# Kernel tuning notes

Hardware: AMD Instinct MI355X
Metric: run time of the kernel (lower is better)

## Reference

```python
import jax, jax.numpy as jnp
import numpy as np
import math

HEAD_DIM = 128
N_HEADS = 32
N_KV_HEADS = 8
ROPE_THETA = 10000.0


def _rotate_half(x):
    x1, x2 = jnp.split(x, 2, axis=-1)
    return jnp.concatenate([-x2, x1], axis=-1)


def _rope_cos_sin(position_ids, head_dim, theta):
    # position_ids: [B, S] int
    inv_freq = 1.0 / (theta ** (jnp.arange(0, head_dim, 2, dtype=jnp.float32) / head_dim))
    freqs = position_ids.astype(jnp.float32)[..., None] * inv_freq[None, None, :]  # [B,S,D/2]
    emb = jnp.concatenate([freqs, freqs], axis=-1)  # [B,S,D]
    return jnp.cos(emb), jnp.sin(emb)


def setup_inputs() -> dict:
    key = jax.random.key(0)
    k1, k2, k3, k4, k5 = jax.random.split(key, 5)
    B, S, H = 1, 2048, 4096
    hidden_states = jax.random.normal(k1, (B, S, H), dtype=jnp.float32)
    Wq = jax.random.normal(k2, (N_HEADS * HEAD_DIM, H), dtype=jnp.float32) * (1.0 / math.sqrt(H))
    Wk = jax.random.normal(k3, (N_KV_HEADS * HEAD_DIM, H), dtype=jnp.float32) * (1.0 / math.sqrt(H))
    Wv = jax.random.normal(k4, (N_KV_HEADS * HEAD_DIM, H), dtype=jnp.float32) * (1.0 / math.sqrt(H))
    Wo = jax.random.normal(k5, (H, N_HEADS * HEAD_DIM), dtype=jnp.float32) * (1.0 / math.sqrt(H))
    position_ids = jnp.arange(S, dtype=jnp.int32)[None, :]
    return {"hidden_states": hidden_states, "Wq": Wq, "Wk": Wk, "Wv": Wv, "Wo": Wo,
            "position_ids": position_ids}


def reference(hidden_states, Wq, Wk, Wv, Wo, position_ids):
    B, S, H = hidden_states.shape
    d = HEAD_DIM
    groups = N_HEADS // N_KV_HEADS

    # projections (torch Linear: x @ W^T)
    q = (hidden_states @ Wq.T).reshape(B, S, N_HEADS, d).transpose(0, 2, 1, 3)      # [B,Hq,S,d]
    k = (hidden_states @ Wk.T).reshape(B, S, N_KV_HEADS, d).transpose(0, 2, 1, 3)   # [B,Hk,S,d]
    v = (hidden_states @ Wv.T).reshape(B, S, N_KV_HEADS, d).transpose(0, 2, 1, 3)

    cos, sin = _rope_cos_sin(position_ids, d, ROPE_THETA)  # [B,S,d]
    cos = cos[:, None, :, :]
    sin = sin[:, None, :, :]
    q = q * cos + _rotate_half(q) * sin
    k = k * cos + _rotate_half(k) * sin

    # GQA: repeat kv heads
    k = jnp.repeat(k, groups, axis=1)  # [B,Hq,S,d]
    v = jnp.repeat(v, groups, axis=1)

    scores = jnp.einsum('bhqd,bhkd->bhqk', q, k) / math.sqrt(d)
    causal = jnp.tril(jnp.ones((S, S), dtype=bool))
    scores = jnp.where(causal[None, None], scores, jnp.finfo(jnp.float32).min)
    attn = jax.nn.softmax(scores.astype(jnp.float32), axis=-1).astype(q.dtype)

    out = jnp.einsum('bhqk,bhkd->bhqd', attn, v)        # [B,Hq,S,d]
    out = out.transpose(0, 2, 1, 3).reshape(B, S, N_HEADS * d)
    return out @ Wo.T
```

## Files before the change

kernel.cpp:

```cpp
#include <hip/hip_runtime.h>
#include <hip/hip_bf16.h>
#include <cstdint>
#include <cstddef>

#define S_LEN 2048
#define HID   4096
#define HD    128
#define NH    32
#define NKV   8
#define KVW   (NKV * HD)
#define QKVN  (HID + 2 * KVW)

typedef __bf16 bf16x8_t __attribute__((ext_vector_type(8)));
typedef float  f32x4_t  __attribute__((ext_vector_type(4)));
typedef unsigned short u16x8_t __attribute__((ext_vector_type(8)));

__device__ __forceinline__ unsigned short f2b(float f) {
  unsigned u = __float_as_uint(f);
  u += 0x7FFFu + ((u >> 16) & 1u);
  return (unsigned short)(u >> 16);
}
__device__ __forceinline__ float b2f(unsigned short v) {
  return __uint_as_float(((unsigned)v) << 16);
}
__device__ __forceinline__ void gld_lds16(const void* g, void* l) {
  __builtin_amdgcn_global_load_lds(
      (const __attribute__((address_space(1))) void*)g,
      (__attribute__((address_space(3))) void*)l, 16, 0, 0);
}

__global__ void cvt_kernel(const float* __restrict__ src,
                           unsigned short* __restrict__ dst, int n4) {
  int i = blockIdx.x * blockDim.x + threadIdx.x;
  int stride = gridDim.x * blockDim.x;
  for (; i < n4; i += stride) {
    float4 v = reinterpret_cast<const float4*>(src)[i];
    ushort4 o;
    o.x = f2b(v.x); o.y = f2b(v.y); o.z = f2b(v.z); o.w = f2b(v.w);
    reinterpret_cast<ushort4*>(dst)[i] = o;
  }
}

__global__ void rope_kernel(unsigned short* __restrict__ Q,
                            unsigned short* __restrict__ Kb,
                            const int* __restrict__ pos_ids) {
  const int total = S_LEN * (NH + NKV) * 64;
  int idx = blockIdx.x * blockDim.x + threadIdx.x;
  int stride = gridDim.x * blockDim.x;
  for (; idx < total; idx += stride) {
    int s   = idx / ((NH + NKV) * 64);
    int rem = idx % ((NH + NKV) * 64);
    int hp  = rem >> 6;
    int i   = rem & 63;
    unsigned short* ptr; int W, h;
    if (hp < NH) { ptr = Q;  W = HID; h = hp; }
    else         { ptr = Kb; W = KVW; h = hp - NH; }
    float pos = (float)pos_ids[s];
    float ang = pos * __expf(-(float)i * 0.14391156516f);
    float sn, cs;
    sincosf(ang, &sn, &cs);
    size_t base = (size_t)s * W + (size_t)h * HD + i;
    float lo = b2f(ptr[base]);
    float hi = b2f(ptr[base + 64]);
    ptr[base]      = f2b(lo * cs - hi * sn);
    ptr[base + 64] = f2b(hi * cs + lo * sn);
  }
}

template <int BM, int MODE>
__global__ __launch_bounds__(512, 2) void gemm8p_kernel(
    const unsigned short* __restrict__ A, const unsigned short* __restrict__ B,
    void* __restrict__ C0, void* __restrict__ C1, void* __restrict__ C2,
    int N, int K) {
  constexpr int BN = 256;
  constexpr int PWM = BM / 2;
  constexpr int MFR = PWM / 16;
  constexpr int MPP = MFR / 4;
  constexpr int ABYTES = BM * 128;
  constexpr int TILE_LDS = ABYTES + BN * 128;
  constexpr int A_UNITS = ABYTES / 8192;
  constexpr int TUNITS = A_UNITS + 4;
  constexpr int VM_N = TUNITS - 2;
  __shared__ char ldsB[2 * TILE_LDS];

  const int tid  = threadIdx.x;
  const int lane = tid & 63;
  const int wid  = tid >> 6;
  const int wm = wid >> 2, wn = wid & 3;
  const int lr = lane & 15, g = lane >> 4;

  const int gx = gridDim.x;
  const int nwg = gx * gridDim.y;
  const int lin = blockIdx.y * gx + blockIdx.x;
  const int swz = (lin & 7) * (nwg >> 3) + (lin >> 3);
  const int bm = (swz / gx) * BM;
  const int bn = (swz % gx) * BN;

  const int nk = K >> 6;
  const int ni = nk >> 1;
  const int xr = (lr & 7) << 4;

  auto stage_u = [&](int t, int u) {
    if (t >= nk) return;
    const int riu = tid >> 3;
    const int cbs = ((tid & 7) << 4) ^ ((riu & 7) << 4);
    const char* src;
    if (u < A_UNITS)
      src = (const char*)A + ((size_t)(bm + u * 64 + riu) * K + t * 64) * 2 + cbs;
    else
      src = (const char*)B + ((size_t)(bn + (u - A_UNITS) * 64 + riu) * K + t * 64) * 2 + cbs;
    gld_lds16(src, ldsB + (t & 1) * TILE_LDS + u * 8192 + tid * 16);
  };

  auto rdA = [&](const char* bb, int m, int k) {
    const int row = wm * PWM + m * 16 + lr;
    return *(const bf16x8_t*)(bb + row * 128 + ((k * 64 + g * 16) ^ xr));
  };
  auto rdB = [&](const char* bb, int n, int k) {
    const int row = wn * 64 + n * 16 + lr;
    return *(const bf16x8_t*)(bb + ABYTES + row * 128 + ((k * 64 + g * 16) ^ xr));
  };

  for (int t = 0; t < 2; ++t)
    for (int u = 0; u < TUNITS; ++u) stage_u(t, u);
  asm volatile("s_waitcnt vmcnt(0)" ::: "memory");
  __builtin_amdgcn_sched_barrier(0);
  __builtin_amdgcn_s_barrier();

  f32x4_t acc[MFR][4];
#pragma unroll
  for (int m = 0; m < MFR; ++m)
#pragma unroll
    for (int n = 0; n < 4; ++n) acc[m][n] = f32x4_t{0.f, 0.f, 0.f, 0.f};

  bf16x8_t bfr[4][2], af[MPP][2];

#define MFMA_BLOCK(MB)                                                        \
  __builtin_amdgcn_s_setprio(1);                                              \
  _Pragma("unroll") for (int m = 0; m < MPP; ++m)                             \
    _Pragma("unroll") for (int n = 0; n < 4; ++n)                             \
      _Pragma("unroll") for (int k = 0; k < 2; ++k)                           \
        acc[(MB) + m][n] = __builtin_amdgcn_mfma_f32_16x16x32_bf16(           \
            af[m][k], bfr[n][k], acc[(MB) + m][n], 0, 0, 0);                  \
  __builtin_amdgcn_s_setprio(0);

#define GATE()                                                                \
  __builtin_amdgcn_s_barrier();                                               \
  asm volatile("s_waitcnt lgkmcnt(0)" ::: "memory");                          \
  __builtin_amdgcn_sched_barrier(0);

  for (int i = 0; i < ni; ++i) {
    const char* baseE = ldsB;
    const char* baseO = ldsB + TILE_LDS;
    const int tO = 2 * i + 1, tE2 = 2 * i + 2, tO2 = 2 * i + 3;
    const bool last = (i == ni - 1);

#pragma unroll
    for (int n = 0; n < 4; ++n)
#pragma unroll
      for (int k = 0; k < 2; ++k) bfr[n][k] = rdB(baseE, n, k);
#pragma unroll
    for (int m = 0; m < MPP; ++m)
#pragma unroll
      for (int k = 0; k < 2; ++k) af[m][k] = rdA(baseE, m, k);
    if (i > 0) {
      if constexpr (BM == 256) { stage_u(tO, 1); stage_u(tO, 3); }
      else                     { stage_u(tO, 0); stage_u(tO, 1); }
    }
    GATE(); MFMA_BLOCK(0);
    __builtin_amdgcn_s_barrier();

#pragma unroll
    for (int m = 0; m < MPP; ++m)
#pragma unroll
      for (int k = 0; k < 2; ++k) af[m][k] = rdA(baseE, MPP + m, k);
    stage_u(tE2, A_UNITS + 0); stage_u(tE2, A_UNITS + 1);
    GATE(); MFMA_BLOCK(MPP);
    __builtin_amdgcn_s_barrier();

#pragma unroll
    for (int m = 0; m < MPP; ++m)
#pragma unroll
      for (int k = 0; k < 2; ++k) af[m][k] = rdA(baseE, 2 * MPP + m, k);
    stage_u(tE2, A_UNITS + 2); stage_u(tE2, A_UNITS + 3);
    GATE(); MFMA_BLOCK(2 * MPP);
    __builtin_amdgcn_s_barrier();

#pragma unroll
    for (int m = 0; m < MPP; ++m)
#pragma unroll
      for (int k = 0; k < 2; ++k) af[m][k] = rdA(baseE, 3 * MPP + m, k);
    if constexpr (BM == 256) { stage_u(tE2, 0); stage_u(tE2, 2); }
    GATE(); MFMA_BLOCK(3 * MPP);
    if (last) { asm volatile("s_waitcnt vmcnt(0)" ::: "memory"); }
    else      { asm volatile("s_waitcnt vmcnt(%0)" :: "n"(VM_N) : "memory"); }
    __builtin_amdgcn_sched_barrier(0);
    __builtin_amdgcn_s_barrier();

#pragma unroll
    for (int n = 0; n < 4; ++n)
#pragma unroll
      for (int k = 0; k < 2; ++k) bfr[n][k] = rdB(baseO, n, k);
#pragma unroll
    for (int m = 0; m < MPP; ++m)
#pragma unroll
      for (int k = 0; k < 2; ++k) af[m][k] = rdA(baseO, m, k);
    if constexpr (BM == 256) { stage_u(tE2, 1); stage_u(tE2, 3); }
    else                     { stage_u(tE2, 0); stage_u(tE2, 1); }
    GATE(); MFMA_BLOCK(0);
    __builtin_amdgcn_s_barrier();

#pragma unroll
    for (int m = 0; m < MPP; ++m)
#pragma unroll
      for (int k = 0; k < 2; ++k) af[m][k] = rdA(baseO, MPP + m, k);
    stage_u(tO2, A_UNITS + 0); stage_u(tO2, A_UNITS + 1);
    GATE(); MFMA_BLOCK(MPP);
    __builtin_amdgcn_s_barrier();

#pragma unroll
    for (int m = 0; m < MPP; ++m)
#pragma unroll
      for (int k = 0; k < 2; ++k) af[m][k] = rdA(baseO, 2 * MPP + m, k);
    stage_u(tO2, A_UNITS + 2); stage_u(tO2, A_UNITS + 3);
    GATE(); MFMA_BLOCK(2 * MPP);
    __builtin_amdgcn_s_barrier();

#pragma unroll
    for (int m = 0; m < MPP; ++m)
#pragma unroll
      for (int k = 0; k < 2; ++k) af[m][k] = rdA(baseO, 3 * MPP + m, k);
    if constexpr (BM == 256) { stage_u(tO2, 0); stage_u(tO2, 2); }
    GATE(); MFMA_BLOCK(3 * MPP);
    if (!last) { asm volatile("s_waitcnt vmcnt(%0)" :: "n"(VM_N) : "memory"); }
    __builtin_amdgcn_sched_barrier(0);
    __builtin_amdgcn_s_barrier();
  }
#undef MFMA_BLOCK
#undef GATE

#pragma unroll
  for (int mf = 0; mf < MFR; ++mf) {
    const int row0 = bm + wm * PWM + mf * 16 + g * 4;
#pragma unroll
    for (int nf = 0; nf < 4; ++nf) {
      const int col = bn + wn * 64 + nf * 16 + lr;
      if constexpr (MODE == 1) {
#pragma unroll
        for (int r = 0; r < 4; ++r)
          ((float*)C0)[(size_t)(row0 + r) * N + col] = acc[mf][nf][r];
      } else {
        if (col < HID) {
#pragma unroll
          for (int r = 0; r < 4; ++r)
            ((unsigned short*)C0)[(size_t)(row0 + r) * HID + col] = f2b(acc[mf][nf][r]);
        } else if (col < HID + KVW) {
#pragma unroll
          for (int r = 0; r < 4; ++r)
            ((unsigned short*)C1)[(size_t)(row0 + r) * KVW + (col - HID)] = f2b(acc[mf][nf][r]);
        } else {
          const int c2 = col - HID - KVW;
          ushort4 w;
          w.x = f2b(acc[mf][nf][0]); w.y = f2b(acc[mf][nf][1]);
          w.z = f2b(acc[mf][nf][2]); w.w = f2b(acc[mf][nf][3]);
          *(ushort4*)(void*)&((unsigned short*)C2)[(size_t)c2 * S_LEN + row0] = w;
        }
      }
    }
  }
}

__global__ __launch_bounds__(256) void attn_kernel(
    const unsigned short* __restrict__ Q, const unsigned short* __restrict__ K,
    const unsigned short* __restrict__ VtG, unsigned short* __restrict__ O) {
  __shared__ unsigned short Kl[64][136];
  __shared__ unsigned short Vt[128][72];
  __shared__ unsigned short Pl[4][16][72];

  const int tid  = threadIdx.x;
  const int lane = tid & 63;
  const int wave = tid >> 6;
  const int h    = blockIdx.y;
  const int kvh  = h >> 2;
  const int pair = blockIdx.x;
  const int lr   = lane & 15;
  const int g    = lane >> 4;
  const int lk8  = g * 8;
  const float scale = 0.08838834764831845f;
  const unsigned short* Vbase = VtG + (size_t)kvh * HD * S_LEN;

  const int ksr = tid >> 4, ksc = (tid & 15) * 8;
  const int vsr = tid >> 3, vsc = (tid & 7) * 8;

  for (int pass = 0; pass < 2; ++pass) {
    const int qb = pass == 0 ? (31 - pair) : pair;
    const int q0 = qb * 64;
    const int qrow = q0 + wave * 16;
    const int nkv = qb + 1;

    bf16x8_t qf[4];
    {
      const unsigned short* qp = Q + (size_t)(qrow + lr) * HID + (size_t)h * HD;
#pragma unroll
      for (int c = 0; c < 4; ++c)
        qf[c] = *(const bf16x8_t*)(const void*)(qp + c * 32 + lk8);
    }
    f32x4_t oacc[8];
#pragma unroll
    for (int c = 0; c < 8; ++c) oacc[c] = f32x4_t{0.f, 0.f, 0.f, 0.f};
    float m_run = -3e38f, l_run = 0.f;

    u16x8_t kr[4], vr[4];
#pragma unroll
    for (int i = 0; i < 4; ++i)
      kr[i] = *(const u16x8_t*)(const void*)(K + (size_t)(ksr + i * 16) * KVW +
                                             (size_t)kvh * HD + ksc);
#pragma unroll
    for (int i = 0; i < 4; ++i)
      vr[i] = *(const u16x8_t*)(const void*)(Vbase + (size_t)(vsr + i * 32) * S_LEN + vsc);

    for (int it = 0; it < nkv; ++it) {
      const int kv0 = it * 64;
      __builtin_amdgcn_s_barrier();
#pragma unroll
      for (int i = 0; i < 4; ++i)
        *(u16x8_t*)(void*)&Kl[ksr + i * 16][ksc] = kr[i];
#pragma unroll
      for (int i = 0; i < 4; ++i)
        *(u16x8_t*)(void*)&Vt[vsr + i * 32][vsc] = vr[i];
      if (it + 1 < nkv) {
        const int kn = kv0 + 64;
#pragma unroll
        for (int i = 0; i < 4; ++i)
          kr[i] = *(const u16x8_t*)(const void*)(K + (size_t)(kn + ksr + i * 16) * KVW +
                                                 (size_t)kvh * HD + ksc);
#pragma unroll
        for (int i = 0; i < 4; ++i)
          vr[i] = *(const u16x8_t*)(const void*)(Vbase + (size_t)(vsr + i * 32) * S_LEN +
                                                 kn + vsc);
      }
      asm volatile("s_waitcnt lgkmcnt(0)" ::: "memory");
      __builtin_amdgcn_sched_barrier(0);
      __builtin_amdgcn_s_barrier();

      f32x4_t sacc[4];
#pragma unroll
      for (int n = 0; n < 4; ++n) sacc[n] = f32x4_t{0.f, 0.f, 0.f, 0.f};
#pragma unroll
      for (int c = 0; c < 4; ++c) {
        bf16x8_t qc = qf[c];
#pragma unroll
        for (int n = 0; n < 4; ++n) {
          bf16x8_t kf = *(const bf16x8_t*)(const void*)&Kl[n * 16 + lr][c * 32 + lk8];
          sacc[n] = __builtin_amdgcn_mfma_f32_16x16x32_bf16(kf, qc, sacc[n], 0, 0, 0);
        }
      }

      const int qg = qrow + lr;
      const bool diag = (it == nkv - 1);
      float p[16];
      float mloc = -3e38f;
#pragma unroll
      for (int n = 0; n < 4; ++n)
#pragma unroll
        for (int r = 0; r < 4; ++r) {
          float x = sacc[n][r] * scale;
          if (diag) {
            int kg = kv0 + n * 16 + g * 4 + r;
            if (kg > qg) x = -3e38f;
          }
          p[n * 4 + r] = x;
          mloc = fmaxf(mloc, x);
        }
      mloc = fmaxf(mloc, __shfl_xor(mloc, 16));
      mloc = fmaxf(mloc, __shfl_xor(mloc, 32));

      if (__any(mloc > m_run + 8.f)) {
        float m_new = fmaxf(m_run, mloc);
        float alpha = __expf(m_run - m_new);
        float a4[4];
#pragma unroll
        for (int r = 0; r < 4; ++r) a4[r] = __shfl(alpha, g * 4 + r);
#pragma unroll
        for (int c = 0; c < 8; ++c)
#pragma unroll
          for (int r = 0; r < 4; ++r) oacc[c][r] *= a4[r];
        l_run *= alpha;
        m_run = m_new;
      }

      float ssum = 0.f;
#pragma unroll
      for (int i = 0; i < 16; ++i) {
        float e = __expf(p[i] - m_run);
        p[i] = e;
        ssum += e;
      }
      ssum += __shfl_xor(ssum, 16);
      ssum += __shfl_xor(ssum, 32);
      l_run += ssum;

#pragma unroll
      for (int n = 0; n < 4; ++n) {
        ushort4 w;
        w.x = f2b(p[n * 4 + 0]); w.y = f2b(p[n * 4 + 1]);
        w.z = f2b(p[n * 4 + 2]); w.w = f2b(p[n * 4 + 3]);
        *(ushort4*)(void*)&Pl[wave][lr][n * 16 + g * 4] = w;
      }

#pragma unroll
      for (int half = 0; half < 2; ++half) {
        bf16x8_t pf = *(const bf16x8_t*)(const void*)&Pl[wave][lr][half * 32 + lk8];
#pragma unroll
        for (int c = 0; c < 8; ++c) {
          bf16x8_t vf = *(const bf16x8_t*)(const void*)&Vt[c * 16 + lr][half * 32 + lk8];
          oacc[c] = __builtin_amdgcn_mfma_f32_16x16x32_bf16(pf, vf, oacc[c], 0, 0, 0);
        }
      }
    }

    float linv[4];
#pragma unroll
    for (int r = 0; r < 4; ++r) linv[r] = 1.f / __shfl(l_run, g * 4 + r);
#pragma unroll
    for (int r = 0; r < 4; ++r) {
      int row = qrow + g * 4 + r;
#pragma unroll
      for (int c = 0; c < 8; ++c)
        O[(size_t)row * HID + (size_t)h * HD + c * 16 + lr] = f2b(oacc[c][r] * linv[r]);
    }
  }
}

extern "C" void kernel_launch(void* const* d_in, const int* in_sizes, int n_in,
                              void* d_out, int out_size, void* d_ws, size_t ws_size,
                              hipStream_t stream) {
  (void)in_sizes; (void)n_in; (void)out_size; (void)ws_size;
  const float* X  = (const float*)d_in[0];
  const float* Wq = (const float*)d_in[1];
  const float* Wk = (const float*)d_in[2];
  const float* Wv = (const float*)d_in[3];
  const float* Wo = (const float*)d_in[4];
  const int*  pos = (const int*)d_in[5];
  float* out = (float*)d_out;

  unsigned short* Xb  = (unsigned short*)d_ws;
  unsigned short* Wqb = Xb  + (size_t)S_LEN * HID;
  unsigned short* Wkb = Wqb + (size_t)HID * HID;
  unsigned short* Wvb = Wkb + (size_t)KVW * HID;
  unsigned short* Wob = Wvb + (size_t)KVW * HID;
  unsigned short* Qb  = Wob + (size_t)HID * HID;
  unsigned short* Kb  = Qb  + (size_t)S_LEN * HID;
  unsigned short* VtB = Kb  + (size_t)S_LEN * KVW;
  unsigned short* AOb = VtB + (size_t)S_LEN * KVW;

  auto cvt = [&](const float* s, unsigned short* d, size_t n) {
    int n4 = (int)(n / 4);
    int grid = (n4 + 255) / 256;
    if (grid > 4096) grid = 4096;
    cvt_kernel<<<grid, 256, 0, stream>>>(s, d, n4);
  };
  cvt(X,  Xb,  (size_t)S_LEN * HID);
  cvt(Wq, Wqb, (size_t)HID * HID);
  cvt(Wk, Wkb, (size_t)KVW * HID);
  cvt(Wv, Wvb, (size_t)KVW * HID);
  cvt(Wo, Wob, (size_t)HID * HID);

  gemm8p_kernel<256, 2><<<dim3(QKVN / 256, S_LEN / 256), 512, 0, stream>>>(
      Xb, Wqb, Qb, Kb, VtB, QKVN, HID);

  rope_kernel<<<2048, 256, 0, stream>>>(Qb, Kb, pos);

  attn_kernel<<<dim3(16, NH), 256, 0, stream>>>(Qb, Kb, VtB, AOb);

  gemm8p_kernel<128, 1><<<dim3(HID / 256, S_LEN / 128), 512, 0, stream>>>(
      AOb, Wob, out, nullptr, nullptr, HID, HID);
}
```

Measured before the change: 334.5 us.

## Retile GEMMs to fixed 256-row M tiles with variable BN

Changes the GEMM template from a variable M-tile with a fixed 256-wide N-tile to a fixed 256-row M-tile with a variable N-tile (192 for QKV, 128 for the output projection), and reworks the staging schedule to fit. The QKV GEMM now launches 32x8 = 256 workgroups, which presumably targets one full wave across the 256 CUs instead of the previous 24x8 grid. The output projection grid changes shape but keeps the same workgroup count. The grouped block swizzle is removed, which may reduce L2 reuse of tiles. The NFR==3 path stages units in a new irregular order, so the vmcnt accounting has to stay correct.

```diff
diff --git a/kernel.cpp b/kernel.cpp
--- a/kernel.cpp
+++ b/kernel.cpp
@@ -67,20 +67,15 @@
   }
 }
 
-template <int BM, int MODE>
+template <int BN, int MODE>
 __global__ __launch_bounds__(512, 2) void gemm8p_kernel(
     const unsigned short* __restrict__ A, const unsigned short* __restrict__ B,
     void* __restrict__ C0, void* __restrict__ C1, void* __restrict__ C2,
     int N, int K) {
-  constexpr int BN = 256;
-  constexpr int PWM = BM / 2;
-  constexpr int MFR = PWM / 16;
-  constexpr int MPP = MFR / 4;
-  constexpr int ABYTES = BM * 128;
+  constexpr int NFR = BN / 64;
+  constexpr int ABYTES = 256 * 128;
   constexpr int TILE_LDS = ABYTES + BN * 128;
-  constexpr int A_UNITS = ABYTES / 8192;
-  constexpr int TUNITS = A_UNITS + 4;
-  constexpr int VM_N = TUNITS - 2;
+  constexpr int VM_N = NFR + 2;
   __shared__ char ldsB[2 * TILE_LDS];
 
   const int tid  = threadIdx.x;
@@ -88,14 +83,8 @@
   const int wid  = tid >> 6;
   const int wm = wid >> 2, wn = wid & 3;
   const int lr = lane & 15, g = lane >> 4;
-
-  const int gx = gridDim.x;
-  const int nwg = gx * gridDim.y;
-  const int lin = blockIdx.y * gx + blockIdx.x;
-  const int swz = (lin & 7) * (nwg >> 3) + (lin >> 3);
-  const int bm = (swz / gx) * BM;
-  const int bn = (swz % gx) * BN;
-
+  const int bm = blockIdx.y * 256;
+  const int bn = blockIdx.x * BN;
   const int nk = K >> 6;
   const int ni = nk >> 1;
   const int xr = (lr & 7) << 4;
@@ -105,40 +94,40 @@
     const int riu = tid >> 3;
     const int cbs = ((tid & 7) << 4) ^ ((riu & 7) << 4);
     const char* src;
-    if (u < A_UNITS)
+    if (u < 4)
       src = (const char*)A + ((size_t)(bm + u * 64 + riu) * K + t * 64) * 2 + cbs;
     else
-      src = (const char*)B + ((size_t)(bn + (u - A_UNITS) * 64 + riu) * K + t * 64) * 2 + cbs;
+      src = (const char*)B + ((size_t)(bn + (u - 4) * 64 + riu) * K + t * 64) * 2 + cbs;
     gld_lds16(src, ldsB + (t & 1) * TILE_LDS + u * 8192 + tid * 16);
   };
 
   auto rdA = [&](const char* bb, int m, int k) {
-    const int row = wm * PWM + m * 16 + lr;
+    const int row = wm * 128 + m * 16 + lr;
     return *(const bf16x8_t*)(bb + row * 128 + ((k * 64 + g * 16) ^ xr));
   };
   auto rdB = [&](const char* bb, int n, int k) {
-    const int row = wn * 64 + n * 16 + lr;
+    const int row = wn * (BN / 4) + n * 16 + lr;
     return *(const bf16x8_t*)(bb + ABYTES + row * 128 + ((k * 64 + g * 16) ^ xr));
   };
 
   for (int t = 0; t < 2; ++t)
-    for (int u = 0; u < TUNITS; ++u) stage_u(t, u);
+    for (int u = 0; u < 4 + NFR; ++u) stage_u(t, u);
   asm volatile("s_waitcnt vmcnt(0)" ::: "memory");
   __builtin_amdgcn_sched_barrier(0);
   __builtin_amdgcn_s_barrier();
 
-  f32x4_t acc[MFR][4];
-#pragma unroll
-  for (int m = 0; m < MFR; ++m)
-#pragma unroll
-    for (int n = 0; n < 4; ++n) acc[m][n] = f32x4_t{0.f, 0.f, 0.f, 0.f};
-
-  bf16x8_t bfr[4][2], af[MPP][2];
+  f32x4_t acc[8][NFR];
+#pragma unroll
+  for (int m = 0; m < 8; ++m)
+#pragma unroll
+    for (int n = 0; n < NFR; ++n) acc[m][n] = f32x4_t{0.f, 0.f, 0.f, 0.f};
+
+  bf16x8_t bfr[NFR][2], af[2][2];
 
 #define MFMA_BLOCK(MB)                                                        \
   __builtin_amdgcn_s_setprio(1);                                              \
-  _Pragma("unroll") for (int m = 0; m < MPP; ++m)                             \
-    _Pragma("unroll") for (int n = 0; n < 4; ++n)                             \
+  _Pragma("unroll") for (int m = 0; m < 2; ++m)                               \
+    _Pragma("unroll") for (int n = 0; n < NFR; ++n)                           \
       _Pragma("unroll") for (int k = 0; k < 2; ++k)                           \
         acc[(MB) + m][n] = __builtin_amdgcn_mfma_f32_16x16x32_bf16(           \
             af[m][k], bfr[n][k], acc[(MB) + m][n], 0, 0, 0);                  \
@@ -148,6 +137,11 @@
   __builtin_amdgcn_s_barrier();                                               \
   asm volatile("s_waitcnt lgkmcnt(0)" ::: "memory");                          \
   __builtin_amdgcn_sched_barrier(0);
+
+#define RD_A2(bb, m0)                                                         \
+  _Pragma("unroll") for (int m = 0; m < 2; ++m)                               \
+    _Pragma("unroll") for (int k = 0; k < 2; ++k)                             \
+      af[m][k] = rdA(bb, (m0) + m, k);
 
   for (int i = 0; i < ni; ++i) {
     const char* baseE = ldsB;
@@ -156,95 +150,70 @@
     const bool last = (i == ni - 1);
 
 #pragma unroll
-    for (int n = 0; n < 4; ++n)
+    for (int n = 0; n < NFR; ++n)
 #pragma unroll
       for (int k = 0; k < 2; ++k) bfr[n][k] = rdB(baseE, n, k);
-#pragma unroll
-    for (int m = 0; m < MPP; ++m)
-#pragma unroll
-      for (int k = 0; k < 2; ++k) af[m][k] = rdA(baseE, m, k);
-    if (i > 0) {
-      if constexpr (BM == 256) { stage_u(tO, 1); stage_u(tO, 3); }
-      else                     { stage_u(tO, 0); stage_u(tO, 1); }
-    }
+    RD_A2(baseE, 0);
+    if (i > 0) { stage_u(tO, 1); stage_u(tO, 3); }
     GATE(); MFMA_BLOCK(0);
     __builtin_amdgcn_s_barrier();
 
-#pragma unroll
-    for (int m = 0; m < MPP; ++m)
-#pragma unroll
-      for (int k = 0; k < 2; ++k) af[m][k] = rdA(baseE, MPP + m, k);
-    stage_u(tE2, A_UNITS + 0); stage_u(tE2, A_UNITS + 1);
-    GATE(); MFMA_BLOCK(MPP);
-    __builtin_amdgcn_s_barrier();
-
-#pragma unroll
-    for (int m = 0; m < MPP; ++m)
-#pragma unroll
-      for (int k = 0; k < 2; ++k) af[m][k] = rdA(baseE, 2 * MPP + m, k);
-    stage_u(tE2, A_UNITS + 2); stage_u(tE2, A_UNITS + 3);
-    GATE(); MFMA_BLOCK(2 * MPP);
-    __builtin_amdgcn_s_barrier();
-
-#pragma unroll
-    for (int m = 0; m < MPP; ++m)
-#pragma unroll
-      for (int k = 0; k < 2; ++k) af[m][k] = rdA(baseE, 3 * MPP + m, k);
-    if constexpr (BM == 256) { stage_u(tE2, 0); stage_u(tE2, 2); }
-    GATE(); MFMA_BLOCK(3 * MPP);
+    RD_A2(baseE, 2);
+    stage_u(tE2, 4); stage_u(tE2, 5);
+    GATE(); MFMA_BLOCK(2);
+    __builtin_amdgcn_s_barrier();
+
+    RD_A2(baseE, 4);
+    if constexpr (NFR == 3) { stage_u(tE2, 6); stage_u(tE2, 0); }
+    else                    { stage_u(tE2, 0); stage_u(tE2, 2); }
+    GATE(); MFMA_BLOCK(4);
+    __builtin_amdgcn_s_barrier();
+
+    RD_A2(baseE, 6);
+    if constexpr (NFR == 3) { stage_u(tE2, 2); }
+    GATE(); MFMA_BLOCK(6);
     if (last) { asm volatile("s_waitcnt vmcnt(0)" ::: "memory"); }
     else      { asm volatile("s_waitcnt vmcnt(%0)" :: "n"(VM_N) : "memory"); }
     __builtin_amdgcn_sched_barrier(0);
     __builtin_amdgcn_s_barrier();
 
 #pragma unroll
-    for (int n = 0; n < 4; ++n)
+    for (int n = 0; n < NFR; ++n)
 #pragma unroll
       for (int k = 0; k < 2; ++k) bfr[n][k] = rdB(baseO, n, k);
-#pragma unroll
-    for (int m = 0; m < MPP; ++m)
-#pragma unroll
-      for (int k = 0; k < 2; ++k) af[m][k] = rdA(baseO, m, k);
-    if constexpr (BM == 256) { stage_u(tE2, 1); stage_u(tE2, 3); }
-    else                     { stage_u(tE2, 0); stage_u(tE2, 1); }
+    RD_A2(baseO, 0);
+    stage_u(tE2, 1); stage_u(tE2, 3);
     GATE(); MFMA_BLOCK(0);
     __builtin_amdgcn_s_barrier();
 
-#pragma unroll
-    for (int m = 0; m < MPP; ++m)
-#pragma unroll
-      for (int k = 0; k < 2; ++k) af[m][k] = rdA(baseO, MPP + m, k);
-    stage_u(tO2, A_UNITS + 0); stage_u(tO2, A_UNITS + 1);
-    GATE(); MFMA_BLOCK(MPP);
-    __builtin_amdgcn_s_barrier();
-
-#pragma unroll
-    for (int m = 0; m < MPP; ++m)
-#pragma unroll
-      for (int k = 0; k < 2; ++k) af[m][k] = rdA(baseO, 2 * MPP + m, k);
-    stage_u(tO2, A_UNITS + 2); stage_u(tO2, A_UNITS + 3);
-    GATE(); MFMA_BLOCK(2 * MPP);
-    __builtin_amdgcn_s_barrier();
-
-#pragma unroll
-    for (int m = 0; m < MPP; ++m)
-#pragma unroll
-      for (int k = 0; k < 2; ++k) af[m][k] = rdA(baseO, 3 * MPP + m, k);
-    if constexpr (BM == 256) { stage_u(tO2, 0); stage_u(tO2, 2); }
-    GATE(); MFMA_BLOCK(3 * MPP);
+    RD_A2(baseO, 2);
+    stage_u(tO2, 4); stage_u(tO2, 5);
+    GATE(); MFMA_BLOCK(2);
+    __builtin_amdgcn_s_barrier();
+
+    RD_A2(baseO, 4);
+    if constexpr (NFR == 3) { stage_u(tO2, 6); stage_u(tO2, 0); }
+    else                    { stage_u(tO2, 0); stage_u(tO2, 2); }
+    GATE(); MFMA_BLOCK(4);
+    __builtin_amdgcn_s_barrier();
+
+    RD_A2(baseO, 6);
+    if constexpr (NFR == 3) { stage_u(tO2, 2); }
+    GATE(); MFMA_BLOCK(6);
     if (!last) { asm volatile("s_waitcnt vmcnt(%0)" :: "n"(VM_N) : "memory"); }
     __builtin_amdgcn_sched_barrier(0);
     __builtin_amdgcn_s_barrier();
   }
 #undef MFMA_BLOCK
 #undef GATE
-
-#pragma unroll
-  for (int mf = 0; mf < MFR; ++mf) {
-    const int row0 = bm + wm * PWM + mf * 16 + g * 4;
-#pragma unroll
-    for (int nf = 0; nf < 4; ++nf) {
-      const int col = bn + wn * 64 + nf * 16 + lr;
+#undef RD_A2
+
+#pragma unroll
+  for (int mf = 0; mf < 8; ++mf) {
+    const int row0 = bm + wm * 128 + mf * 16 + g * 4;
+#pragma unroll
+    for (int nf = 0; nf < NFR; ++nf) {
+      const int col = bn + wn * (BN / 4) + nf * 16 + lr;
       if constexpr (MODE == 1) {
 #pragma unroll
         for (int r = 0; r < 4; ++r)
@@ -466,13 +435,13 @@
   cvt(Wv, Wvb, (size_t)KVW * HID);
   cvt(Wo, Wob, (size_t)HID * HID);
 
-  gemm8p_kernel<256, 2><<<dim3(QKVN / 256, S_LEN / 256), 512, 0, stream>>>(
+  gemm8p_kernel<192, 2><<<dim3(QKVN / 192, S_LEN / 256), 512, 0, stream>>>(
       Xb, Wqb, Qb, Kb, VtB, QKVN, HID);
 
   rope_kernel<<<2048, 256, 0, stream>>>(Qb, Kb, pos);
 
   attn_kernel<<<dim3(16, NH), 256, 0, stream>>>(Qb, Kb, VtB, AOb);
 
-  gemm8p_kernel<128, 1><<<dim3(HID / 256, S_LEN / 128), 512, 0, stream>>>(
+  gemm8p_kernel<128, 1><<<dim3(HID / 128, S_LEN / 256), 512, 0, stream>>>(
       AOb, Wob, out, nullptr, nullptr, HID, HID);
 }
```

Result: faster. 308.1 us (-7.9%).
